# Optimization experiments

Measured on AMD Instinct MI355X. Metric: run time of the kernel, lower is better.

Reference implementation:

```python
import jax, jax.numpy as jnp
import numpy as np

FIVE = 6            # top-k features kept per output unit
OUT, IN, HID, B = 512, 1024, 32, 256


def setup_inputs() -> dict:
    key = jax.random.key(0)
    ks = jax.random.split(key, 6)
    return {
        "inputs": jax.random.normal(ks[0], (B, IN), jnp.float32),
        "mask": jax.random.normal(ks[1], (OUT, IN), jnp.float32),
        "W1": jax.random.normal(ks[2], (OUT, IN, HID), jnp.float32) / 2.236,
        "W2": jax.random.normal(ks[3], (OUT, HID, HID), jnp.float32) / HID ** 0.5,
        "W3": jax.random.normal(ks[4], (OUT, HID, HID), jnp.float32) / HID ** 0.5,
        "W4": jax.random.normal(ks[5], (OUT, HID, 1), jnp.float32) / HID ** 0.5,
    }


def reference(inputs, mask, W1, W2, W3, W4):
    # top-k binary mask: 1 at the FIVE largest entries of each row of mask
    _, idx = jax.lax.top_k(mask, FIVE)                       # (out, FIVE)
    rows = jnp.arange(mask.shape[0])[:, None]
    m = jnp.zeros_like(mask).at[rows, idx].set(1.0)          # (out, in)

    # gated inputs, broadcast of torch's bmm outer-product trick:
    # x[o,b,i] = inputs[b,i] * m[o,i]
    x = inputs[None, :, :] * m[:, None, :]                   # (out, batch, in)

    # per-output-unit 4-layer MLP (batched over 'o')
    h = jax.nn.relu(jnp.einsum('obi,oih->obh', x, W1))       # (out, batch, hid)
    h = jax.nn.relu(jnp.einsum('obh,ohk->obk', h, W2))
    h = jax.nn.relu(jnp.einsum('obh,ohk->obk', h, W3))
    y = jnp.einsum('obh,oh->ob', h, W4[:, :, 0])             # (out, batch)
    y = jax.nn.sigmoid(y).T                                  # (batch, out)

    # STE binarize (forward value)
    q = (y >= 0.5).astype(y.dtype) * 2.0 - 1.0
    return q
```

## Files before the change

kernel.cpp:

```cpp
#include <hip/hip_runtime.h>
#include <math.h>

#define NOUT 512
#define NIN  1024
#define HID  32
#define NB   256
#define TOPK 6
#define HSTR 40

typedef _Float16 f16x8 __attribute__((ext_vector_type(8)));
typedef float    f32x4 __attribute__((ext_vector_type(4)));

union HU  { _Float16 h; unsigned short u; };
union H4U { _Float16 h[4]; unsigned long long u; };
union H8U { _Float16 h[8]; uint4 u; };

__device__ __forceinline__ unsigned short f16bits(float v) {
    HU c; c.h = (_Float16)v; return c.u;
}

__global__ __launch_bounds__(256) void topk_kernel(
    const float* __restrict__ mask, int* __restrict__ sidx_out)
{
    const int o = (blockIdx.x << 2) | (threadIdx.x >> 6);
    const int l = threadIdx.x & 63;
    const float* mrow = mask + (size_t)o * NIN;

    float v[16];
#pragma unroll
    for (int j = 0; j < 16; ++j) v[j] = mrow[j * 64 + l];

#pragma unroll
    for (int it = 0; it < TOPK; ++it) {
        float bv = v[0]; int bi = l;
#pragma unroll
        for (int j = 1; j < 16; ++j)
            if (v[j] > bv) { bv = v[j]; bi = j * 64 + l; }
#pragma unroll
        for (int off = 32; off; off >>= 1) {
            float ov = __shfl_down(bv, off);
            int   oi = __shfl_down(bi, off);
            if (ov > bv) { bv = ov; bi = oi; }
        }
        bi = __shfl(bi, 0);
#pragma unroll
        for (int j = 0; j < 16; ++j)
            if (bi == j * 64 + l) v[j] = -INFINITY;
        if (l == 0) sidx_out[o * 8 + it] = bi;
    }
}

template<int NMT>
__device__ __forceinline__ void mfma_layer(
    const unsigned short* WtHi, const unsigned short* WtLo,
    const unsigned short* HHi,  const unsigned short* HLo,
    int lane15, int quad, int wb, f32x4 acc[NMT][4])
{
    f16x8 aH[NMT], aL[NMT], bH[4], bL[4];
#pragma unroll
    for (int mt = 0; mt < NMT; ++mt) {
        int off = (mt * 16 + lane15) * HSTR + quad * 8;
        aH[mt] = *(const f16x8*)&WtHi[off];
        aL[mt] = *(const f16x8*)&WtLo[off];
    }
#pragma unroll
    for (int nt = 0; nt < 4; ++nt) {
        int off = (wb + nt * 16 + lane15) * HSTR + quad * 8;
        bH[nt] = *(const f16x8*)&HHi[off];
        bL[nt] = *(const f16x8*)&HLo[off];
    }
#pragma unroll
    for (int mt = 0; mt < NMT; ++mt)
#pragma unroll
        for (int nt = 0; nt < 4; ++nt) {
            acc[mt][nt] = __builtin_amdgcn_mfma_f32_16x16x32_f16(aH[mt], bH[nt], acc[mt][nt], 0, 0, 0);
            acc[mt][nt] = __builtin_amdgcn_mfma_f32_16x16x32_f16(aH[mt], bL[nt], acc[mt][nt], 0, 0, 0);
            acc[mt][nt] = __builtin_amdgcn_mfma_f32_16x16x32_f16(aL[mt], bH[nt], acc[mt][nt], 0, 0, 0);
            acc[mt][nt] = __builtin_amdgcn_mfma_f32_16x16x32_f16(aL[mt], bL[nt], acc[mt][nt], 0, 0, 0);
        }
}

__device__ __forceinline__ void store_h(
    unsigned short* HHi, unsigned short* HLo,
    int lane15, int quad, int wb, f32x4 acc[2][4])
{
#pragma unroll
    for (int mt = 0; mt < 2; ++mt)
#pragma unroll
        for (int nt = 0; nt < 4; ++nt) {
            H4U hi, lo;
#pragma unroll
            for (int r = 0; r < 4; ++r) {
                float v = acc[mt][nt][r];
                v = v > 0.0f ? v : 0.0f;
                _Float16 h = (_Float16)v;
                hi.h[r] = h;
                lo.h[r] = (_Float16)(v - (float)h);
            }
            int off = (wb + nt * 16 + lane15) * HSTR + mt * 16 + quad * 4;
            *(unsigned long long*)&HHi[off] = hi.u;
            *(unsigned long long*)&HLo[off] = lo.u;
        }
}

__global__ __launch_bounds__(128, 4) void mlp_kernel(
    const float* __restrict__ inputs,
    const float* __restrict__ W1,
    const float* __restrict__ W2,
    const float* __restrict__ W3,
    const float* __restrict__ W4,
    const int*   __restrict__ sidxg,
    float* __restrict__ out)
{
    const int o    = blockIdx.x >> 1;
    const int half = (blockIdx.x & 1) << 7;
    const int t    = threadIdx.x;
    const int l = t & 63, lane15 = l & 15, quad = l >> 4;
    const int wb = (t >> 6) << 6;

    __shared__ __align__(16) unsigned short HtHi[128 * HSTR];
    __shared__ __align__(16) unsigned short HtLo[128 * HSTR];
    __shared__ __align__(16) unsigned short WHi[3][HID * HSTR];
    __shared__ __align__(16) unsigned short WLo[3][HID * HSTR];
    __shared__ __align__(16) unsigned short W4Hi[16 * HSTR];
    __shared__ __align__(16) unsigned short W4Lo[16 * HSTR];

    int sj[TOPK];
#pragma unroll
    for (int j = 0; j < TOPK; ++j)
        sj[j] = __builtin_amdgcn_readfirstlane(sidxg[o * 8 + j]);

    const int bglob = half + t;
    float xg[TOPK];
#pragma unroll
    for (int j = 0; j < TOPK; ++j)
        xg[j] = inputs[(size_t)bglob * NIN + sj[j]];

    const float* W1g = W1 + (size_t)o * NIN * HID;
    const float* W2g = W2 + (size_t)o * HID * HID;
    const float* W3g = W3 + (size_t)o * HID * HID;
    const float* W4g = W4 + (size_t)o * HID;

#pragma unroll
    for (int i = 0; i < 8; ++i) {
        int e = t + i * 128, m = e & 31, k = e >> 5;
        float v = (k < TOPK) ? W1g[(size_t)sj[k] * HID + m] : 0.0f;
        _Float16 h = (_Float16)v;
        WHi[0][m * HSTR + k] = f16bits(v);
        WLo[0][m * HSTR + k] = f16bits(v - (float)h);
    }
#pragma unroll
    for (int i = 0; i < 8; ++i) {
        int e = t + i * 128, m = e & 31, k = e >> 5;
        float v2 = W2g[e], v3 = W3g[e];
        _Float16 h2 = (_Float16)v2, h3 = (_Float16)v3;
        WHi[1][m * HSTR + k] = f16bits(v2);
        WLo[1][m * HSTR + k] = f16bits(v2 - (float)h2);
        WHi[2][m * HSTR + k] = f16bits(v3);
        WLo[2][m * HSTR + k] = f16bits(v3 - (float)h3);
    }
#pragma unroll
    for (int i = 0; i < 4; ++i) {
        int e = t + i * 128, m = e >> 5, k = e & 31;
        float v = (m == 0) ? W4g[k] : 0.0f;
        _Float16 h = (_Float16)v;
        W4Hi[m * HSTR + k] = f16bits(v);
        W4Lo[m * HSTR + k] = f16bits(v - (float)h);
    }

    {
        H8U xh, xl;
#pragma unroll
        for (int j = 0; j < 8; ++j) { xh.h[j] = (_Float16)0.0f; xl.h[j] = (_Float16)0.0f; }
#pragma unroll
        for (int j = 0; j < TOPK; ++j) {
            float v = xg[j];
            _Float16 h = (_Float16)v;
            xh.h[j] = h;
            xl.h[j] = (_Float16)(v - (float)h);
        }
        *(uint4*)&HtHi[t * HSTR]      = xh.u;
        *(uint4*)&HtLo[t * HSTR]      = xl.u;
        uint4 z = make_uint4(0, 0, 0, 0);
        *(uint4*)&HtHi[t * HSTR + 8]  = z;
        *(uint4*)&HtHi[t * HSTR + 16] = z;
        *(uint4*)&HtHi[t * HSTR + 24] = z;
        *(uint4*)&HtLo[t * HSTR + 8]  = z;
        *(uint4*)&HtLo[t * HSTR + 16] = z;
        *(uint4*)&HtLo[t * HSTR + 24] = z;
    }
    __syncthreads();

    f32x4 acc[2][4];
#pragma unroll
    for (int L = 0; L < 3; ++L) {
#pragma unroll
        for (int mt = 0; mt < 2; ++mt)
#pragma unroll
            for (int nt = 0; nt < 4; ++nt) acc[mt][nt] = (f32x4){0.f, 0.f, 0.f, 0.f};
        mfma_layer<2>(&WHi[L][0], &WLo[L][0], HtHi, HtLo, lane15, quad, wb, acc);
        store_h(HtHi, HtLo, lane15, quad, wb, acc);
    }

    f32x4 acc4[1][4];
#pragma unroll
    for (int nt = 0; nt < 4; ++nt) acc4[0][nt] = (f32x4){0.f, 0.f, 0.f, 0.f};
    mfma_layer<1>(W4Hi, W4Lo, HtHi, HtLo, lane15, quad, wb, acc4);

    if (quad == 0) {
#pragma unroll
        for (int nt = 0; nt < 4; ++nt) {
            int b = half + wb + nt * 16 + lane15;
            out[(size_t)b * NOUT + o] = (acc4[0][nt][0] >= 0.0f) ? 1.0f : -1.0f;
        }
    }
}

extern "C" void kernel_launch(void* const* d_in, const int* in_sizes, int n_in,
                              void* d_out, int out_size, void* d_ws, size_t ws_size,
                              hipStream_t stream) {
    const float* inputs = (const float*)d_in[0];
    const float* mask   = (const float*)d_in[1];
    const float* W1     = (const float*)d_in[2];
    const float* W2     = (const float*)d_in[3];
    const float* W3     = (const float*)d_in[4];
    const float* W4     = (const float*)d_in[5];
    float* out  = (float*)d_out;
    int*   sidx = (int*)d_ws;

    topk_kernel<<<dim3(NOUT / 4), dim3(256), 0, stream>>>(mask, sidx);
    mlp_kernel<<<dim3(NOUT * 2), dim3(128), 0, stream>>>(
        inputs, W1, W2, W3, W4, sidx, out);
}
```

Before: 115.4 us.

## Transpose inputs in prep kernel and process full batch per output block

The top-k kernel also transposes inputs into a workspace buffer, so the per-unit gather of selected feature columns becomes coalesced reads across the batch. The MLP kernel now uses one 256-thread block per output unit instead of two 128-thread halves, so each unit's weights are staged and split into hi/lo halves only once. Weight staging is rewritten with vectorized float4 loads and 64-bit shared stores. The extra transpose pass adds global traffic, and the larger blocks use twice the shared memory per block, which may lower occupancy.

```diff
diff --git a/kernel.cpp b/kernel.cpp
--- a/kernel.cpp
+++ b/kernel.cpp
@@ -19,34 +19,60 @@
     HU c; c.h = (_Float16)v; return c.u;
 }
 
-__global__ __launch_bounds__(256) void topk_kernel(
-    const float* __restrict__ mask, int* __restrict__ sidx_out)
-{
-    const int o = (blockIdx.x << 2) | (threadIdx.x >> 6);
-    const int l = threadIdx.x & 63;
-    const float* mrow = mask + (size_t)o * NIN;
-
-    float v[16];
-#pragma unroll
-    for (int j = 0; j < 16; ++j) v[j] = mrow[j * 64 + l];
-
-#pragma unroll
-    for (int it = 0; it < TOPK; ++it) {
-        float bv = v[0]; int bi = l;
-#pragma unroll
-        for (int j = 1; j < 16; ++j)
-            if (v[j] > bv) { bv = v[j]; bi = j * 64 + l; }
-#pragma unroll
-        for (int off = 32; off; off >>= 1) {
-            float ov = __shfl_down(bv, off);
-            int   oi = __shfl_down(bi, off);
-            if (ov > bv) { bv = ov; bi = oi; }
-        }
-        bi = __shfl(bi, 0);
-#pragma unroll
-        for (int j = 0; j < 16; ++j)
-            if (bi == j * 64 + l) v[j] = -INFINITY;
-        if (l == 0) sidx_out[o * 8 + it] = bi;
+__global__ __launch_bounds__(256) void prep_kernel(
+    const float* __restrict__ mask,
+    const float* __restrict__ inputs,
+    int*   __restrict__ sidx_out,
+    float* __restrict__ inputsT)
+{
+    __shared__ float tile[64 * 65];
+    const int t = threadIdx.x;
+
+    if (blockIdx.x < 128) {
+        const int o = (blockIdx.x << 2) | (t >> 6);
+        const int l = t & 63;
+        const float* mrow = mask + (size_t)o * NIN;
+
+        float v[16];
+#pragma unroll
+        for (int j = 0; j < 16; ++j) v[j] = mrow[j * 64 + l];
+
+#pragma unroll
+        for (int it = 0; it < TOPK; ++it) {
+            float bv = v[0]; int bi = l;
+#pragma unroll
+            for (int j = 1; j < 16; ++j)
+                if (v[j] > bv) { bv = v[j]; bi = j * 64 + l; }
+#pragma unroll
+            for (int off = 32; off; off >>= 1) {
+                float ov = __shfl_down(bv, off);
+                int   oi = __shfl_down(bi, off);
+                if (ov > bv) { bv = ov; bi = oi; }
+            }
+            bi = __shfl(bi, 0);
+#pragma unroll
+            for (int j = 0; j < 16; ++j)
+                if (bi == j * 64 + l) v[j] = -INFINITY;
+            if (l == 0) sidx_out[o * 8 + it] = bi;
+        }
+    } else {
+        const int bid = blockIdx.x - 128;
+        const int rt = bid >> 2;
+        const int ct = bid & 3;
+        const int il = t & 63;
+        const int ql = t >> 6;
+
+#pragma unroll
+        for (int it = 0; it < 16; ++it) {
+            int bl = ql + it * 4;
+            tile[bl * 65 + il] = inputs[(size_t)(ct * 64 + bl) * NIN + rt * 64 + il];
+        }
+        __syncthreads();
+#pragma unroll
+        for (int it = 0; it < 16; ++it) {
+            int iw = ql + it * 4;
+            inputsT[(size_t)(rt * 64 + iw) * NB + ct * 64 + il] = tile[il * 65 + iw];
+        }
     }
 }
 
@@ -103,8 +129,8 @@
         }
 }
 
-__global__ __launch_bounds__(128, 4) void mlp_kernel(
-    const float* __restrict__ inputs,
+__global__ __launch_bounds__(256, 2) void mlp_kernel(
+    const float* __restrict__ inputsT,
     const float* __restrict__ W1,
     const float* __restrict__ W2,
     const float* __restrict__ W3,
@@ -112,14 +138,13 @@
     const int*   __restrict__ sidxg,
     float* __restrict__ out)
 {
-    const int o    = blockIdx.x >> 1;
-    const int half = (blockIdx.x & 1) << 7;
-    const int t    = threadIdx.x;
+    const int o = blockIdx.x;
+    const int t = threadIdx.x;
     const int l = t & 63, lane15 = l & 15, quad = l >> 4;
     const int wb = (t >> 6) << 6;
 
-    __shared__ __align__(16) unsigned short HtHi[128 * HSTR];
-    __shared__ __align__(16) unsigned short HtLo[128 * HSTR];
+    __shared__ __align__(16) unsigned short HtHi[NB * HSTR];
+    __shared__ __align__(16) unsigned short HtLo[NB * HSTR];
     __shared__ __align__(16) unsigned short WHi[3][HID * HSTR];
     __shared__ __align__(16) unsigned short WLo[3][HID * HSTR];
     __shared__ __align__(16) unsigned short W4Hi[16 * HSTR];
@@ -130,42 +155,56 @@
     for (int j = 0; j < TOPK; ++j)
         sj[j] = __builtin_amdgcn_readfirstlane(sidxg[o * 8 + j]);
 
-    const int bglob = half + t;
     float xg[TOPK];
 #pragma unroll
     for (int j = 0; j < TOPK; ++j)
-        xg[j] = inputs[(size_t)bglob * NIN + sj[j]];
+        xg[j] = inputsT[(size_t)sj[j] * NB + t];
 
     const float* W1g = W1 + (size_t)o * NIN * HID;
     const float* W2g = W2 + (size_t)o * HID * HID;
     const float* W3g = W3 + (size_t)o * HID * HID;
     const float* W4g = W4 + (size_t)o * HID;
 
-#pragma unroll
-    for (int i = 0; i < 8; ++i) {
-        int e = t + i * 128, m = e & 31, k = e >> 5;
-        float v = (k < TOPK) ? W1g[(size_t)sj[k] * HID + m] : 0.0f;
+    {
+        const int m = t >> 3, kg = t & 7;
+        H4U hi, lo;
+#pragma unroll
+        for (int r = 0; r < 4; ++r) {
+            int k = kg * 4 + r;
+            float v = (k < TOPK) ? W1g[(size_t)sj[k] * HID + m] : 0.0f;
+            _Float16 h = (_Float16)v;
+            hi.h[r] = h;
+            lo.h[r] = (_Float16)(v - (float)h);
+        }
+        *(unsigned long long*)&WHi[0][m * HSTR + kg * 4] = hi.u;
+        *(unsigned long long*)&WLo[0][m * HSTR + kg * 4] = lo.u;
+    }
+
+    {
+        const int k = t >> 3, m0 = (t & 7) * 4;
+        float4 v2 = *(const float4*)&W2g[t * 4];
+        float4 v3 = *(const float4*)&W3g[t * 4];
+        const float a2[4] = {v2.x, v2.y, v2.z, v2.w};
+        const float a3[4] = {v3.x, v3.y, v3.z, v3.w};
+#pragma unroll
+        for (int r = 0; r < 4; ++r) {
+            _Float16 h2 = (_Float16)a2[r], h3 = (_Float16)a3[r];
+            WHi[1][(m0 + r) * HSTR + k] = f16bits(a2[r]);
+            WLo[1][(m0 + r) * HSTR + k] = f16bits(a2[r] - (float)h2);
+            WHi[2][(m0 + r) * HSTR + k] = f16bits(a3[r]);
+            WLo[2][(m0 + r) * HSTR + k] = f16bits(a3[r] - (float)h3);
+        }
+    }
+
+    if (t < HSTR) {
+        float v = (t < HID) ? W4g[t] : 0.0f;
         _Float16 h = (_Float16)v;
-        WHi[0][m * HSTR + k] = f16bits(v);
-        WLo[0][m * HSTR + k] = f16bits(v - (float)h);
-    }
-#pragma unroll
-    for (int i = 0; i < 8; ++i) {
-        int e = t + i * 128, m = e & 31, k = e >> 5;
-        float v2 = W2g[e], v3 = W3g[e];
-        _Float16 h2 = (_Float16)v2, h3 = (_Float16)v3;
-        WHi[1][m * HSTR + k] = f16bits(v2);
-        WLo[1][m * HSTR + k] = f16bits(v2 - (float)h2);
-        WHi[2][m * HSTR + k] = f16bits(v3);
-        WLo[2][m * HSTR + k] = f16bits(v3 - (float)h3);
-    }
-#pragma unroll
-    for (int i = 0; i < 4; ++i) {
-        int e = t + i * 128, m = e >> 5, k = e & 31;
-        float v = (m == 0) ? W4g[k] : 0.0f;
-        _Float16 h = (_Float16)v;
-        W4Hi[m * HSTR + k] = f16bits(v);
-        W4Lo[m * HSTR + k] = f16bits(v - (float)h);
+        W4Hi[t] = f16bits(v);
+        W4Lo[t] = f16bits(v - (float)h);
+    }
+    for (int idx = HSTR + t; idx < 16 * HSTR; idx += 256) {
+        W4Hi[idx] = 0;
+        W4Lo[idx] = 0;
     }
 
     {
@@ -210,7 +249,7 @@
     if (quad == 0) {
 #pragma unroll
         for (int nt = 0; nt < 4; ++nt) {
-            int b = half + wb + nt * 16 + lane15;
+            int b = wb + nt * 16 + lane15;
             out[(size_t)b * NOUT + o] = (acc4[0][nt][0] >= 0.0f) ? 1.0f : -1.0f;
         }
     }
@@ -227,8 +266,9 @@
     const float* W4     = (const float*)d_in[5];
     float* out  = (float*)d_out;
     int*   sidx = (int*)d_ws;
-
-    topk_kernel<<<dim3(NOUT / 4), dim3(256), 0, stream>>>(mask, sidx);
-    mlp_kernel<<<dim3(NOUT * 2), dim3(128), 0, stream>>>(
-        inputs, W1, W2, W3, W4, sidx, out);
-}
+    float* inputsT = (float*)((char*)d_ws + 16384);
+
+    prep_kernel<<<dim3(192), dim3(256), 0, stream>>>(mask, inputs, sidx, inputsT);
+    mlp_kernel<<<dim3(NOUT), dim3(256), 0, stream>>>(
+        inputsT, W1, W2, W3, W4, sidx, out);
+}
```

Result: faster. 111.0 us (-3.8%).
